# Performance work log

Measured on AMD Instinct MI355X. Metric: run time of the kernel, lower is better.

The kernel has to match this reference:

```python
import jax, jax.numpy as jnp
import numpy as np

B = 128      # batch
HW = 224     # image height/width
P = 16       # patch size
D = 512      # token_dim
NH = 8       # n_heads
L = 6        # t_blocks
M = 2048     # mlp_layer_size
NC = 10      # output classes
GP = HW // P            # patches per side
T = GP * GP + 1         # tokens incl. class token (197)
EPS = 1e-5


def _ln(x, g, b):
    m = jnp.mean(x, axis=-1, keepdims=True)
    v = jnp.mean(jnp.square(x - m), axis=-1, keepdims=True)
    return (x - m) / jnp.sqrt(v + EPS) * g + b


def setup_inputs() -> dict:
    key = jax.random.key(0)
    ks = iter(jax.random.split(key, 32))
    s = 0.02
    inp = {
        "images": jax.random.normal(next(ks), (B, 1, HW, HW), dtype=jnp.float32),
        "lin_map_w": jax.random.normal(next(ks), (D, P * P), dtype=jnp.float32) * s,
        "lin_map_b": jnp.zeros((D,), jnp.float32),
        "class_token": jax.random.uniform(next(ks), (1, D), dtype=jnp.float32),
        "ln1_g": jnp.ones((L, D), jnp.float32),
        "ln1_b": jnp.zeros((L, D), jnp.float32),
        "ln2_g": jnp.ones((L, D), jnp.float32),
        "ln2_b": jnp.zeros((L, D), jnp.float32),
        "qw": jax.random.normal(next(ks), (L, NH, D, D), dtype=jnp.float32) * s,
        "qb": jnp.zeros((L, NH, D), jnp.float32),
        "kw": jax.random.normal(next(ks), (L, NH, D, D), dtype=jnp.float32) * s,
        "kb": jnp.zeros((L, NH, D), jnp.float32),
        "vw": jax.random.normal(next(ks), (L, NH, D, D), dtype=jnp.float32) * s,
        "vb": jnp.zeros((L, NH, D), jnp.float32),
        "map_w": jax.random.normal(next(ks), (L, T, T * NH), dtype=jnp.float32) * s,
        "map_b": jnp.zeros((L, T), jnp.float32),
        "mlp_w1": jax.random.normal(next(ks), (L, M, D), dtype=jnp.float32) * s,
        "mlp_b1": jnp.zeros((L, M), jnp.float32),
        "mlp_w2": jax.random.normal(next(ks), (L, D, M), dtype=jnp.float32) * s,
        "mlp_b2": jnp.zeros((L, D), jnp.float32),
        "cls_w": jax.random.normal(next(ks), (NC, D), dtype=jnp.float32) * s,
        "cls_b": jnp.zeros((NC,), jnp.float32),
    }
    return inp


def reference(images, lin_map_w, lin_map_b, class_token, ln1_g, ln1_b, ln2_g, ln2_b,
              qw, qb, kw, kb, vw, vb, map_w, map_b,
              mlp_w1, mlp_b1, mlp_w2, mlp_b2, cls_w, cls_b):
    n = images.shape[0]
    img = images[:, 0]  # (B, HW, HW), channel squeezed as in patching_func
    # non-overlapping patch extraction (patchify with step=patch_size)
    patches = img.reshape(n, GP, P, GP, P).transpose(0, 1, 3, 2, 4).reshape(n, GP * GP, P * P)
    emb = patches @ lin_map_w.T + lin_map_b                 # (B, nP, D)
    cls = jnp.broadcast_to(class_token, (n, 1, D))
    x = jnp.concatenate([cls, emb], axis=1)                 # (B, T, D)
    scale = 1.0 / np.sqrt(T - 1)                            # quirky scale from source
    for l in range(L):
        h = _ln(x, ln1_g[l], ln1_b[l])
        q = jnp.einsum('btd,hed->bhte', h, qw[l]) + qb[l][None, :, None, :]
        k = jnp.einsum('btd,hed->bhte', h, kw[l]) + kb[l][None, :, None, :]
        v = jnp.einsum('btd,hed->bhte', h, vw[l]) + vb[l][None, :, None, :]
        attn = jax.nn.softmax(jnp.einsum('bhte,bhse->bhts', q, k) * scale, axis=-1)
        av = jnp.einsum('bhts,bhse->bhte', attn, v)         # (B, NH, T, D)
        res = av.reshape(n, NH * T, D)                      # head-major concat along tokens
        msa = jnp.einsum('bmd,tm->btd', res, map_w[l]) + map_b[l][None, :, None]
        x = x + msa
        y = _ln(x, ln2_g[l], ln2_b[l])
        mlp = jax.nn.gelu(y @ mlp_w1[l].T + mlp_b1[l], approximate=False) @ mlp_w2[l].T + mlp_b2[l]
        x = y + mlp                                         # note: residual uses ln2(x), per source
    logits = x[:, 0] @ cls_w.T + cls_b
    return jax.nn.softmax(logits, axis=-1)
```

## Files before the change

### kernel.cpp

```cpp
#include <hip/hip_runtime.h>
#include <hip/hip_bf16.h>
#include <math.h>

#define B_   128
#define HW_  224
#define P_   16
#define D_   512
#define NH_  8
#define L_   6
#define M_   2048
#define NC_  10
#define GP_  14
#define T_   197
#define TP_  224
#define EPS_ 1e-5f
#define ZVW2_ 2048
#define RCW_ 448

typedef __hip_bfloat16 bf16;
typedef __attribute__((ext_vector_type(8))) __bf16 bf16x8;
typedef __attribute__((ext_vector_type(4))) float  f32x4;

__device__ __forceinline__ void gload16(const void* g, void* l) {
    __builtin_amdgcn_global_load_lds(
        (const __attribute__((address_space(1))) void*)g,
        (__attribute__((address_space(3))) void*)l, 16, 0, 0);
}


__global__ void k_f32_to_bf16v(const float* __restrict__ in, bf16* __restrict__ out, long n8) {
    long stride = (long)gridDim.x * blockDim.x;
    for (long i = (long)blockIdx.x * blockDim.x + threadIdx.x; i < n8; i += stride) {
        float4 a = ((const float4*)in)[i * 2], b = ((const float4*)in)[i * 2 + 1];
        union { uint4 u; bf16 h[8]; } r;
        r.h[0] = __float2bfloat16(a.x); r.h[1] = __float2bfloat16(a.y);
        r.h[2] = __float2bfloat16(a.z); r.h[3] = __float2bfloat16(a.w);
        r.h[4] = __float2bfloat16(b.x); r.h[5] = __float2bfloat16(b.y);
        r.h[6] = __float2bfloat16(b.z); r.h[7] = __float2bfloat16(b.w);
        ((uint4*)out)[i] = r.u;
    }
}

__global__ void k_f32_to_bf16v2(const float* __restrict__ in1, bf16* __restrict__ out1,
                                const float* __restrict__ in2, bf16* __restrict__ out2, long n8) {
    long stride = (long)gridDim.x * blockDim.x;
    for (long i = (long)blockIdx.x * blockDim.x + threadIdx.x; i < n8; i += stride) {
        {
            float4 a = ((const float4*)in1)[i * 2], b = ((const float4*)in1)[i * 2 + 1];
            union { uint4 u; bf16 h[8]; } r;
            r.h[0] = __float2bfloat16(a.x); r.h[1] = __float2bfloat16(a.y);
            r.h[2] = __float2bfloat16(a.z); r.h[3] = __float2bfloat16(a.w);
            r.h[4] = __float2bfloat16(b.x); r.h[5] = __float2bfloat16(b.y);
            r.h[6] = __float2bfloat16(b.z); r.h[7] = __float2bfloat16(b.w);
            ((uint4*)out1)[i] = r.u;
        }
        {
            float4 a = ((const float4*)in2)[i * 2], b = ((const float4*)in2)[i * 2 + 1];
            union { uint4 u; bf16 h[8]; } r;
            r.h[0] = __float2bfloat16(a.x); r.h[1] = __float2bfloat16(a.y);
            r.h[2] = __float2bfloat16(a.z); r.h[3] = __float2bfloat16(a.w);
            r.h[4] = __float2bfloat16(b.x); r.h[5] = __float2bfloat16(b.y);
            r.h[6] = __float2bfloat16(b.z); r.h[7] = __float2bfloat16(b.w);
            ((uint4*)out2)[i] = r.u;
        }
    }
}

__global__ void k_prep_wv(const float* __restrict__ vw, bf16* __restrict__ wzv) {
    int idx = blockIdx.x * blockDim.x + threadIdx.x;
    if (idx >= NH_ * D_ * (D_ / 8)) return;
    int d8 = idx & 63;
    int e  = (idx >> 6) & 511;
    int h  = idx >> 15;
    long so = ((long)(h * D_ + e)) * D_ + d8 * 8;
    float4 a = *(const float4*)(vw + so), b = *(const float4*)(vw + so + 4);
    union { uint4 u; bf16 hh[8]; } rr;
    rr.hh[0] = __float2bfloat16(a.x); rr.hh[1] = __float2bfloat16(a.y);
    rr.hh[2] = __float2bfloat16(a.z); rr.hh[3] = __float2bfloat16(a.w);
    rr.hh[4] = __float2bfloat16(b.x); rr.hh[5] = __float2bfloat16(b.y);
    rr.hh[6] = __float2bfloat16(b.z); rr.hh[7] = __float2bfloat16(b.w);
    ((uint4*)wzv)[((long)(h * 1024 + 512 + e)) * 64 + d8] = rr.u;
}

__global__ void k_prep_ub(const float* __restrict__ kw, const float* __restrict__ qb,
                          const float* __restrict__ vb, float* __restrict__ out) {
    int idx = blockIdx.x * blockDim.x + threadIdx.x;
    if (idx >= NH_ * 1024) return;
    int j = idx & 1023, h = idx >> 10;
    if (j < 512) {
        const float* kwh = kw + (long)h * D_ * D_ + j;
        const float* qbh = qb + h * D_;
        float s = 0.f;
        for (int e = 0; e < D_; e++) s += kwh[(long)e * D_] * qbh[e];
        out[idx] = s;
    } else {
        out[idx] = vb[h * D_ + (j - 512)];
    }
}

__global__ void k_patchify(const float* __restrict__ img, bf16* __restrict__ patches) {
    long idx = (long)blockIdx.x * blockDim.x + threadIdx.x;
    long total = (long)B_ * 196 * 256;
    if (idx >= total) return;
    int q = (int)(idx & 255);
    int p = (int)((idx >> 8) % 196);
    int b = (int)(idx / (196 * 256));
    int gy = p / GP_, gx = p % GP_;
    int py = q >> 4,  px = q & 15;
    patches[idx] = __float2bfloat16(img[((long)b * HW_ + gy * P_ + py) * HW_ + gx * P_ + px]);
}

__global__ void k_cls_token(const float* __restrict__ tok, float* __restrict__ x) {
    int i = blockIdx.x * blockDim.x + threadIdx.x;
    if (i < B_ * D_) {
        int b = i >> 9, d = i & 511;
        x[(long)b * T_ * D_ + d] = tok[d];
    }
}

__global__ void k_prep_map(const float* __restrict__ in, bf16* __restrict__ out) {
    int idx = blockIdx.x * blockDim.x + threadIdx.x;
    int total = NH_ * T_ * TP_;
    if (idx >= total) return;
    int s = idx % TP_;
    int t = (idx / TP_) % T_;
    int h = idx / (TP_ * T_);
    float v = (s < T_) ? in[t * (T_ * NH_) + h * T_ + s] : 0.f;
    out[idx] = __float2bfloat16(v);
}


template<int WRITE_Y>
__global__ __launch_bounds__(256) void k_ln(const float* x,
        const float* __restrict__ g, const float* __restrict__ bb,
        bf16* __restrict__ obf, float* of, int rows) {
    int wid = blockIdx.x * 4 + (threadIdx.x >> 6);
    if (wid >= rows) return;
    int lane = threadIdx.x & 63;
    const float* xr = x + (long)wid * D_;
    float v[8];
    float s = 0.f;
#pragma unroll
    for (int i = 0; i < 8; i++) { v[i] = xr[i * 64 + lane]; s += v[i]; }
#pragma unroll
    for (int off = 32; off; off >>= 1) s += __shfl_xor(s, off, 64);
    float mean = s * (1.f / D_);
    float sq = 0.f;
#pragma unroll
    for (int i = 0; i < 8; i++) { float d = v[i] - mean; sq += d * d; }
#pragma unroll
    for (int off = 32; off; off >>= 1) sq += __shfl_xor(sq, off, 64);
    float inv = rsqrtf(sq * (1.f / D_) + EPS_);
#pragma unroll
    for (int i = 0; i < 8; i++) {
        int d = i * 64 + lane;
        float val = (v[i] - mean) * inv * g[d] + bb[d];
        obf[(long)wid * D_ + d] = __float2bfloat16(val);
        if (WRITE_Y) of[(long)wid * D_ + d] = val;
    }
}


__global__ __launch_bounds__(256) void k_attn_ssm2(
        const bf16* __restrict__ Qbase, long ldq, long qImg, long qHead,
        const bf16* __restrict__ Kbase, long ldk, long kImg,
        bf16* __restrict__ Pm, float scale) {
    __shared__ __align__(16) bf16 Qs[128][32];
    __shared__ __align__(16) bf16 Ks[256][32];
    int z = blockIdx.z;
    int img = z & 127, h2 = z >> 7;
    int q0 = blockIdx.y * 128;
    int tid = threadIdx.x;
    int wv = tid >> 6, lane = tid & 63;

    const bf16* Qp = Qbase + (long)img * qImg + (long)h2 * qHead;
    const bf16* Kp = Kbase + (long)img * kImg;

    int sRow = 16 * wv + (lane >> 2);
    int sCol = (lane & 3) * 8;
    const bf16* gQ = Qp + (long)(q0 + sRow) * ldq + sCol;
    const bf16* gK = Kp + (long)sRow * ldk + sCol;
    char* lQ = (char*)Qs + (16 * wv) * 64;
    char* lK = (char*)Ks + (16 * wv) * 64;

    f32x4 acc[2][13];
#pragma unroll
    for (int j = 0; j < 2; j++)
#pragma unroll
        for (int f = 0; f < 13; f++) acc[j][f] = (f32x4){0.f, 0.f, 0.f, 0.f};

    for (int kt = 0; kt < 16; kt++) {
        long k0 = (long)kt * 32;
        gload16(gQ + k0, lQ);
        gload16(gQ + 64 * ldq + k0, lQ + 4096);
#pragma unroll
        for (int p = 0; p < 4; p++)
            gload16(gK + (long)(p * 64) * ldk + k0, lK + p * 4096);
        __syncthreads();
        bf16x8 af[2];
#pragma unroll
        for (int j = 0; j < 2; j++)
            af[j] = *(const bf16x8*)&Qs[wv * 32 + j * 16 + (lane & 15)][(lane >> 4) * 8];
#pragma unroll
        for (int f = 0; f < 13; f++) {
            bf16x8 bfr = *(const bf16x8*)&Ks[f * 16 + (lane & 15)][(lane >> 4) * 8];
            acc[0][f] = __builtin_amdgcn_mfma_f32_16x16x32_bf16(af[0], bfr, acc[0][f], 0, 0, 0);
            acc[1][f] = __builtin_amdgcn_mfma_f32_16x16x32_bf16(af[1], bfr, acc[1][f], 0, 0, 0);
        }
        __syncthreads();
    }

    int c1 = lane & 15, grp = lane >> 4;
    const bf16 z0 = __float2bfloat16(0.f);
#pragma unroll
    for (int j = 0; j < 2; j++) {
        float mx[4] = {-1e30f, -1e30f, -1e30f, -1e30f};
        float sm[4] = {0.f, 0.f, 0.f, 0.f};
#pragma unroll
        for (int f = 0; f < 13; f++) {
            bool val = (f * 16 + c1 < T_);
#pragma unroll
            for (int r = 0; r < 4; r++) {
                float v = val ? acc[j][f][r] * scale : -1e30f;
                acc[j][f][r] = v;
                mx[r] = fmaxf(mx[r], v);
            }
        }
#pragma unroll
        for (int r = 0; r < 4; r++)
#pragma unroll
            for (int off = 1; off < 16; off <<= 1) mx[r] = fmaxf(mx[r], __shfl_xor(mx[r], off, 64));
#pragma unroll
        for (int f = 0; f < 13; f++) {
            bool val = (f * 16 + c1 < T_);
#pragma unroll
            for (int r = 0; r < 4; r++) {
                float e = val ? expf(acc[j][f][r] - mx[r]) : 0.f;
                acc[j][f][r] = e;
                sm[r] += e;
            }
        }
#pragma unroll
        for (int r = 0; r < 4; r++) {
#pragma unroll
            for (int off = 1; off < 16; off <<= 1) sm[r] += __shfl_xor(sm[r], off, 64);
            sm[r] = 1.f / sm[r];
        }
#pragma unroll
        for (int r = 0; r < 4; r++) {
            int qi = q0 + wv * 32 + j * 16 + grp * 4 + r;
            if (qi >= T_) continue;
            bf16* prow = Pm + ((long)z * T_ + qi) * TP_;
#pragma unroll
            for (int f = 0; f < 13; f++)
                prow[f * 16 + c1] = __float2bfloat16(acc[j][f][r] * sm[r]);
            prow[208 + c1] = z0;
        }
    }
}


__device__ __forceinline__ float geluf(float v) {
    return 0.5f * v * (1.f + erff(v * 0.70710678118654752f));
}

template<int MODE, bool GUARD, bool SWZ>
__global__ __launch_bounds__(256) void k_gemm_bt(
        const bf16* __restrict__ A, long lda, long bsA,
        const bf16* __restrict__ Bw, long ldb, long bsB,
        void* __restrict__ Cp, long ldc, long bsC,
        const float* __restrict__ bias,
        const float* res, long ldres,
        int Mt, int Nt, int Kt) {
    __shared__ __align__(16) bf16 As[128][32];
    __shared__ __align__(16) bf16 Bs[128][32];
    int bz = blockIdx.z;
    A  += (long)bz * bsA;
    Bw += (long)bz * bsB;

    unsigned bx = blockIdx.x, by = blockIdx.y;
    if (SWZ) {
        unsigned nx = gridDim.x;
        unsigned nwg = nx * gridDim.y;
        unsigned f = by * nx + bx;
        unsigned q = nwg >> 3, r = nwg & 7;
        unsigned xcd = f & 7, idx = f >> 3;
        unsigned base = (xcd < r) ? xcd * (q + 1) : r * (q + 1) + (xcd - r) * q;
        unsigned nf = base + idx;
        bx = nf % nx;
        by = nf / nx;
    }
    int m0 = by * 128, n0 = bx * 128;

    int tid = threadIdx.x;
    int wv = tid >> 6, lane = tid & 63;
    int wm = (wv >> 1) * 64, wn = (wv & 1) * 64;
    int lrow = lane & 15, koff = (lane >> 4) * 8;

    int rA = tid >> 2, pA = (tid & 3) * 8;
    const bf16* gA0 = A  + (long)(m0 + rA) * lda + pA;
    const bf16* gA1 = A  + (long)(m0 + 64 + rA) * lda + pA;
    const bf16* gB0 = Bw + (long)(n0 + rA) * ldb + pA;
    const bf16* gB1 = Bw + (long)(n0 + 64 + rA) * ldb + pA;
    char* lA0 = (char*)As + (wv * 64) * 16;
    char* lA1 = (char*)As + (256 + wv * 64) * 16;
    char* lB0 = (char*)Bs + (wv * 64) * 16;
    char* lB1 = (char*)Bs + (256 + wv * 64) * 16;

    f32x4 acc[4][4];
#pragma unroll
    for (int i = 0; i < 4; i++)
#pragma unroll
        for (int j = 0; j < 4; j++) acc[i][j] = (f32x4){0.f, 0.f, 0.f, 0.f};

    int kTiles = Kt >> 5;
    for (int kt = 0; kt < kTiles; kt++) {
        long k0 = (long)kt << 5;
        gload16(gA0 + k0, lA0);
        gload16(gA1 + k0, lA1);
        gload16(gB0 + k0, lB0);
        gload16(gB1 + k0, lB1);
        __syncthreads();
        bf16x8 af[4], bfr[4];
#pragma unroll
        for (int mi = 0; mi < 4; mi++) af[mi]  = *(const bf16x8*)&As[wm + mi * 16 + lrow][koff];
#pragma unroll
        for (int ni = 0; ni < 4; ni++) bfr[ni] = *(const bf16x8*)&Bs[wn + ni * 16 + lrow][koff];
#pragma unroll
        for (int mi = 0; mi < 4; mi++)
#pragma unroll
            for (int ni = 0; ni < 4; ni++)
                acc[mi][ni] = __builtin_amdgcn_mfma_f32_16x16x32_bf16(af[mi], bfr[ni], acc[mi][ni], 0, 0, 0);
        __syncthreads();
    }

    int r4 = (lane >> 4) * 4, c1 = lane & 15;
    float bv[4];
#pragma unroll
    for (int ni = 0; ni < 4; ni++) {
        int col = n0 + wn + ni * 16 + c1;
        bv[ni] = (bias && (!GUARD || col < Nt)) ? bias[col] : 0.f;
    }
#pragma unroll
    for (int mi = 0; mi < 4; mi++) {
#pragma unroll
        for (int r = 0; r < 4; r++) {
            int row = m0 + wm + mi * 16 + r4 + r;
            if (GUARD && row >= Mt) continue;
            long base = (long)bz * bsC + (long)row * ldc + n0 + wn + c1;
#pragma unroll
            for (int ni = 0; ni < 4; ni++) {
                if (GUARD && (n0 + wn + ni * 16 + c1) >= Nt) continue;
                float v = acc[mi][ni][r] + bv[ni];
                long cidx = base + ni * 16;
                if (MODE == 0)      ((float*)Cp)[cidx] = v;
                else if (MODE == 1) ((bf16*)Cp)[cidx]  = __float2bfloat16(v);
                else if (MODE == 2) ((bf16*)Cp)[cidx]  = __float2bfloat16(geluf(v));
                else                ((float*)Cp)[cidx] = v + res[(long)row * ldres + n0 + wn + c1 + ni * 16];
            }
        }
    }
}

__global__ __launch_bounds__(256) void k_gemm_r(
        const bf16* __restrict__ mapPair,
        const bf16* __restrict__ Pb,
        bf16* __restrict__ Rcat) {
    __shared__ __align__(16) bf16 As[128][32];
    __shared__ __align__(16) bf16 Bs[128][32];
    int z = blockIdx.z;
    int img = z & 127, h2 = z >> 7;
    const bf16* A  = mapPair + (long)h2 * T_ * TP_;
    const bf16* Bw = Pb + ((long)(h2 * 128 + img)) * (long)T_ * TP_;
    bf16* Cp = Rcat + (long)img * 224 * RCW_ + h2 * 224;
    int m0 = blockIdx.y * 128, n0 = blockIdx.x * 128;
    int tid = threadIdx.x;
    int wv = tid >> 6, lane = tid & 63;
    int wm = (wv >> 1) * 64, wn = (wv & 1) * 64;
    int lrow = lane & 15, koff = (lane >> 4) * 8;

    int rA = tid >> 2, pA = (tid & 3) * 8;
    const bf16* gA0 = A + (long)(m0 + rA) * TP_ + pA;
    const bf16* gA1 = A + (long)(m0 + 64 + rA) * TP_ + pA;
    char* lA0 = (char*)As + (wv * 64) * 16;
    char* lA1 = (char*)As + (256 + wv * 64) * 16;
    int bk = tid & 31, bg = tid >> 5;

    f32x4 acc[4][4];
#pragma unroll
    for (int i = 0; i < 4; i++)
#pragma unroll
        for (int j = 0; j < 4; j++) acc[i][j] = (f32x4){0.f, 0.f, 0.f, 0.f};

    for (int kt = 0; kt < 7; kt++) {
        long k0 = (long)kt << 5;
        gload16(gA0 + k0, lA0);
        gload16(gA1 + k0, lA1);
#pragma unroll
        for (int i = 0; i < 2; i++) {
            int g = bg + 8 * i;
            uint4 v = *(const uint4*)(Bw + (k0 + bk) * TP_ + n0 + g * 8);
            const bf16* pv = (const bf16*)&v;
#pragma unroll
            for (int j = 0; j < 8; j++) Bs[g * 8 + j][bk] = pv[j];
        }
        __syncthreads();
        bf16x8 af[4], bfr[4];
#pragma unroll
        for (int mi = 0; mi < 4; mi++) af[mi]  = *(const bf16x8*)&As[wm + mi * 16 + lrow][koff];
#pragma unroll
        for (int ni = 0; ni < 4; ni++) bfr[ni] = *(const bf16x8*)&Bs[wn + ni * 16 + lrow][koff];
#pragma unroll
        for (int mi = 0; mi < 4; mi++)
#pragma unroll
            for (int ni = 0; ni < 4; ni++)
                acc[mi][ni] = __builtin_amdgcn_mfma_f32_16x16x32_bf16(af[mi], bfr[ni], acc[mi][ni], 0, 0, 0);
        __syncthreads();
    }

    int r4 = (lane >> 4) * 4, c1 = lane & 15;
#pragma unroll
    for (int mi = 0; mi < 4; mi++) {
#pragma unroll
        for (int r = 0; r < 4; r++) {
            int row = m0 + wm + mi * 16 + r4 + r;
            if (row >= T_) continue;
#pragma unroll
            for (int ni = 0; ni < 4; ni++) {
                int col = n0 + wn + ni * 16 + c1;
                if (col >= 224) continue;
                Cp[(long)row * RCW_ + col] = __float2bfloat16(acc[mi][ni][r]);
            }
        }
    }
}

__global__ __launch_bounds__(256) void k_gemm_rv(
        const bf16* __restrict__ Rcat,
        const bf16* __restrict__ ZV,
        float* __restrict__ xf,
        const float* __restrict__ rowbias) {
    __shared__ __align__(16) bf16 As[128][32];
    __shared__ __align__(16) bf16 Bs[128][32];
    int img = blockIdx.z;
    const bf16* A = Rcat + (long)img * 224 * RCW_;
    const bf16* Vimg = ZV + (long)img * T_ * ZVW2_;
    float* Cp = xf + (long)img * T_ * D_;
    int m0 = blockIdx.y * 128, n0 = blockIdx.x * 128;
    int tid = threadIdx.x;
    int wv = tid >> 6, lane = tid & 63;
    int wm = (wv >> 1) * 64, wn = (wv & 1) * 64;
    int lrow = lane & 15, koff = (lane >> 4) * 8;

    int rA = tid >> 2, pA = (tid & 3) * 8;
    const bf16* gA0 = A + (long)(m0 + rA) * RCW_ + pA;
    const bf16* gA1 = A + (long)(m0 + 64 + rA) * RCW_ + pA;
    char* lA0 = (char*)As + (wv * 64) * 16;
    char* lA1 = (char*)As + (256 + wv * 64) * 16;
    int bk = tid & 31, bg = tid >> 5;

    f32x4 acc[4][4];
#pragma unroll
    for (int i = 0; i < 4; i++)
#pragma unroll
        for (int j = 0; j < 4; j++) acc[i][j] = (f32x4){0.f, 0.f, 0.f, 0.f};

    for (int kt = 0; kt < 14; kt++) {
        long k0 = (long)kt << 5;
        gload16(gA0 + k0, lA0);
        gload16(gA1 + k0, lA1);
        const bf16* Vb = (kt < 7) ? (Vimg + 512 + k0 * ZVW2_)
                                  : (Vimg + 1536 + (k0 - 224) * ZVW2_);
#pragma unroll
        for (int i = 0; i < 2; i++) {
            int g = bg + 8 * i;
            uint4 v = *(const uint4*)(Vb + (long)bk * ZVW2_ + n0 + g * 8);
            const bf16* pv = (const bf16*)&v;
#pragma unroll
            for (int j = 0; j < 8; j++) Bs[g * 8 + j][bk] = pv[j];
        }
        __syncthreads();
        bf16x8 af[4], bfr[4];
#pragma unroll
        for (int mi = 0; mi < 4; mi++) af[mi]  = *(const bf16x8*)&As[wm + mi * 16 + lrow][koff];
#pragma unroll
        for (int ni = 0; ni < 4; ni++) bfr[ni] = *(const bf16x8*)&Bs[wn + ni * 16 + lrow][koff];
#pragma unroll
        for (int mi = 0; mi < 4; mi++)
#pragma unroll
            for (int ni = 0; ni < 4; ni++)
                acc[mi][ni] = __builtin_amdgcn_mfma_f32_16x16x32_bf16(af[mi], bfr[ni], acc[mi][ni], 0, 0, 0);
        __syncthreads();
    }

    int r4 = (lane >> 4) * 4, c1 = lane & 15;
#pragma unroll
    for (int mi = 0; mi < 4; mi++) {
#pragma unroll
        for (int r = 0; r < 4; r++) {
            int row = m0 + wm + mi * 16 + r4 + r;
            if (row >= T_) continue;
            float rb = rowbias ? rowbias[row] : 0.f;
#pragma unroll
            for (int ni = 0; ni < 4; ni++) {
                int col = n0 + wn + ni * 16 + c1;
                Cp[(long)row * D_ + col] += acc[mi][ni][r] + rb * 0.25f;
            }
        }
    }
}

__global__ __launch_bounds__(256) void k_gemm_tn(
        const bf16* __restrict__ A, long lda, long bsA,
        const bf16* __restrict__ Bw, long ldb, long bsB,
        bf16* __restrict__ Cp, long ldc, long bsC,
        int Mt, int Nt, int Kt) {
    __shared__ __align__(16) bf16 As[128][32];
    __shared__ __align__(16) bf16 Bs[128][32];
    int bz = blockIdx.z;
    A  += (long)bz * bsA;
    Bw += (long)bz * bsB;
    int m0 = blockIdx.y * 128, n0 = blockIdx.x * 128;
    int tid = threadIdx.x;
    int wv = tid >> 6, lane = tid & 63;
    int wm = (wv >> 1) * 64, wn = (wv & 1) * 64;
    int lrow = lane & 15, koff = (lane >> 4) * 8;
    int bk = tid & 31, bg = tid >> 5;

    f32x4 acc[4][4];
#pragma unroll
    for (int i = 0; i < 4; i++)
#pragma unroll
        for (int j = 0; j < 4; j++) acc[i][j] = (f32x4){0.f, 0.f, 0.f, 0.f};

    int kTiles = Kt >> 5;
    for (int kt = 0; kt < kTiles; kt++) {
        long k0 = (long)kt << 5;
#pragma unroll
        for (int i = 0; i < 2; i++) {
            int g = bg + 8 * i;
            uint4 va = *(const uint4*)(A + (k0 + bk) * lda + m0 + g * 8);
            const bf16* pa = (const bf16*)&va;
#pragma unroll
            for (int j = 0; j < 8; j++) As[g * 8 + j][bk] = pa[j];
            uint4 vb = *(const uint4*)(Bw + (k0 + bk) * ldb + n0 + g * 8);
            const bf16* pb = (const bf16*)&vb;
#pragma unroll
            for (int j = 0; j < 8; j++) Bs[g * 8 + j][bk] = pb[j];
        }
        __syncthreads();
        bf16x8 af[4], bfr[4];
#pragma unroll
        for (int mi = 0; mi < 4; mi++) af[mi]  = *(const bf16x8*)&As[wm + mi * 16 + lrow][koff];
#pragma unroll
        for (int ni = 0; ni < 4; ni++) bfr[ni] = *(const bf16x8*)&Bs[wn + ni * 16 + lrow][koff];
#pragma unroll
        for (int mi = 0; mi < 4; mi++)
#pragma unroll
            for (int ni = 0; ni < 4; ni++)
                acc[mi][ni] = __builtin_amdgcn_mfma_f32_16x16x32_bf16(af[mi], bfr[ni], acc[mi][ni], 0, 0, 0);
        __syncthreads();
    }

    int r4 = (lane >> 4) * 4, c1 = lane & 15;
#pragma unroll
    for (int mi = 0; mi < 4; mi++) {
#pragma unroll
        for (int r = 0; r < 4; r++) {
            int row = m0 + wm + mi * 16 + r4 + r;
            if (row >= Mt) continue;
#pragma unroll
            for (int ni = 0; ni < 4; ni++) {
                int col = n0 + wn + ni * 16 + c1;
                if (col >= Nt) continue;
                Cp[(long)bz * bsC + (long)row * ldc + col] = __float2bfloat16(acc[mi][ni][r]);
            }
        }
    }
}


__global__ __launch_bounds__(64) void k_classifier(const float* __restrict__ x,
        const float* __restrict__ w, const float* __restrict__ bias, float* __restrict__ out) {
    int b = blockIdx.x, lane = threadIdx.x;
    const float* xr = x + (long)b * T_ * D_;
    float logits[NC_];
#pragma unroll
    for (int c = 0; c < NC_; c++) {
        float s = 0.f;
        for (int d = lane; d < D_; d += 64) s += xr[d] * w[c * D_ + d];
#pragma unroll
        for (int off = 32; off; off >>= 1) s += __shfl_xor(s, off, 64);
        logits[c] = s + bias[c];
    }
    float mx = -1e30f;
#pragma unroll
    for (int c = 0; c < NC_; c++) mx = fmaxf(mx, logits[c]);
    float sum = 0.f;
#pragma unroll
    for (int c = 0; c < NC_; c++) { float e = expf(logits[c] - mx); logits[c] = e; sum += e; }
    if (lane == 0) {
        float inv = 1.f / sum;
#pragma unroll
        for (int c = 0; c < NC_; c++) out[(long)b * NC_ + c] = logits[c] * inv;
    }
}


extern "C" void kernel_launch(void* const* d_in, const int* in_sizes, int n_in,
                              void* d_out, int out_size, void* d_ws, size_t ws_size,
                              hipStream_t stream) {
    const float* images  = (const float*)d_in[0];
    const float* lin_w   = (const float*)d_in[1];
    const float* lin_b   = (const float*)d_in[2];
    const float* cls_tok = (const float*)d_in[3];
    const float* ln1_g   = (const float*)d_in[4];
    const float* ln1_b   = (const float*)d_in[5];
    const float* ln2_g   = (const float*)d_in[6];
    const float* ln2_b   = (const float*)d_in[7];
    const float* qw      = (const float*)d_in[8];
    const float* qb      = (const float*)d_in[9];
    const float* kw      = (const float*)d_in[10];
    const float* kb      = (const float*)d_in[11];
    const float* vw      = (const float*)d_in[12];
    const float* vb      = (const float*)d_in[13];
    const float* map_w   = (const float*)d_in[14];
    const float* map_b   = (const float*)d_in[15];
    const float* w1      = (const float*)d_in[16];
    const float* b1      = (const float*)d_in[17];
    const float* w2      = (const float*)d_in[18];
    const float* b2      = (const float*)d_in[19];
    const float* cls_w   = (const float*)d_in[20];
    const float* cls_b   = (const float*)d_in[21];

    char* wp = (char*)d_ws;
    auto alloc = [&](size_t bytes) { char* p = wp; wp += (bytes + 255) & ~(size_t)255; return p; };
    const long BT = (long)B_ * T_;

    float* xf   = (float*)alloc(BT * D_ * 4);
    bf16*  hb   = (bf16*) alloc((BT + 192) * D_ * 2);
    bf16*  ZVh2 = (bf16*) alloc((size_t)(BT + 160) * ZVW2_ * 2);
    bf16*  m1c  = ZVh2;
    bf16*  Pb2  = (bf16*) alloc(((size_t)256 * T_ + 64) * TP_ * 2);
    char*  rcReg= alloc(((size_t)128 * 224 + 64) * RCW_ * 2);
    bf16*  Rcat = (bf16*)rcReg;
    bf16*  patches = (bf16*)rcReg;
    bf16*  wqb  = (bf16*)rcReg;
    bf16*  wkb  = (bf16*)(rcReg + (long)NH_ * D_ * D_ * 2);
    bf16*  wzv  = (bf16*) alloc(((long)NH_ * 1024 + 64) * D_ * 2);
    float* zvb  = (float*)alloc((long)NH_ * 1024 * 4);
    bf16*  wmapP= (bf16*) alloc(((long)NH_ * T_ + 64) * TP_ * 2);
    bf16*  w1l  = (bf16*) alloc((long)(M_ + 64) * D_ * 2);
    bf16*  w2l  = (bf16*) alloc((long)(D_ + 64) * M_ * 2);
    bf16*  wlin = (bf16*) alloc((long)(D_ + 64) * 256 * 2);

    k_f32_to_bf16v<<<1024, 256, 0, stream>>>(lin_w, wlin, (long)D_ * 256 / 8);
    {
        long tot = (long)B_ * 196 * 256;
        k_patchify<<<(int)((tot + 255) / 256), 256, 0, stream>>>(images, patches);
        k_cls_token<<<(B_ * D_ + 255) / 256, 256, 0, stream>>>(cls_tok, xf);
        k_gemm_bt<0, true, false><<<dim3(4, 2, B_), 256, 0, stream>>>(
            patches, 256, (long)196 * 256,
            wlin, 256, 0,
            xf + D_, D_, (long)T_ * D_,
            lin_b, nullptr, 0,
            196, D_, 256);
    }

    const float scale = 1.0f / 14.0f;
    const int lnGrid = (int)((BT + 3) / 4);

    for (int l = 0; l < L_; l++) {
        k_f32_to_bf16v2<<<1024, 256, 0, stream>>>(
            qw + (long)l * NH_ * D_ * D_, wqb,
            kw + (long)l * NH_ * D_ * D_, wkb, (long)NH_ * D_ * D_ / 8);
        k_gemm_tn<<<dim3(4, 4, NH_), 256, 0, stream>>>(
            wkb, D_, (long)D_ * D_,
            wqb, D_, (long)D_ * D_,
            wzv, D_, (long)1024 * D_,
            D_, D_, D_);
        k_prep_wv<<<(NH_ * D_ * (D_ / 8) + 255) / 256, 256, 0, stream>>>(
            vw + (long)l * NH_ * D_ * D_, wzv);
        k_prep_ub<<<(NH_ * 1024 + 255) / 256, 256, 0, stream>>>(
            kw + (long)l * NH_ * D_ * D_, qb + (long)l * NH_ * D_,
            vb + (long)l * NH_ * D_, zvb);
        k_f32_to_bf16v2<<<1024, 256, 0, stream>>>(
            w1 + (long)l * M_ * D_, w1l,
            w2 + (long)l * D_ * M_, w2l, (long)M_ * D_ / 8);
        k_prep_map<<<(NH_ * T_ * TP_ + 255) / 256, 256, 0, stream>>>(
            map_w + (long)l * T_ * T_ * NH_, wmapP);

        k_ln<0><<<lnGrid, 256, 0, stream>>>(xf, ln1_g + l * D_, ln1_b + l * D_, hb, nullptr, (int)BT);

        for (int hp = 0; hp < 4; hp++) {
            k_gemm_bt<1, false, true><<<dim3(16, 197, 1), 256, 0, stream>>>(
                hb, D_, 0, wzv + (long)hp * 2048 * D_, D_, 0,
                ZVh2, ZVW2_, 0, zvb + (long)hp * 2048, nullptr, 0,
                (int)BT, ZVW2_, D_);

            k_attn_ssm2<<<dim3(1, 2, 256), 256, 0, stream>>>(
                ZVh2, ZVW2_, (long)T_ * ZVW2_, 1024,
                hb, D_, (long)T_ * D_,
                Pb2, scale);

            k_gemm_r<<<dim3(2, 2, 256), 256, 0, stream>>>(
                wmapP + (long)(hp * 2) * T_ * TP_, Pb2, Rcat);

            k_gemm_rv<<<dim3(4, 2, B_), 256, 0, stream>>>(
                Rcat, ZVh2, xf, map_b + (long)l * T_);
        }

        k_ln<1><<<lnGrid, 256, 0, stream>>>(xf, ln2_g + l * D_, ln2_b + l * D_, hb, xf, (int)BT);

        k_gemm_bt<2, false, true><<<dim3(16, 197, 1), 256, 0, stream>>>(
            hb, D_, 0, w1l, D_, 0,
            m1c, M_, 0, b1 + (long)l * M_, nullptr, 0, (int)BT, M_, D_);
        k_gemm_bt<3, false, true><<<dim3(4, 197, 1), 256, 0, stream>>>(
            m1c, M_, 0, w2l, M_, 0,
            xf, D_, 0, b2 + (long)l * D_, xf, D_, (int)BT, D_, M_);
    }

    k_classifier<<<B_, 64, 0, stream>>>(xf, cls_w, cls_b, (float*)d_out);
}
```

Measured before the change: 7.700 ms.

## Add 256x256-tile double-buffered GEMM kernel for QKV and MLP projections

Introduces a new 512-thread GEMM kernel that uses 256x256 output tiles with K-step 64, double-buffered LDS filled via direct global-to-LDS loads, XOR-swizzled LDS layout, an XCD-aware workgroup remap, and s_setprio around the MFMA bursts. It replaces the older 128-tile GEMM for the Z/V projection, MLP up (GELU) and MLP down (residual) GEMMs. The larger tiles are meant to raise data reuse per tile and hide load latency. The M dimension is padded to 25344 rows with no bounds guard, so several buffers are enlarged to absorb out-of-range reads and writes. The bigger tile also reduces the number of workgroups and raises register and LDS pressure per block.

Result: slower. 8.166 ms (+6.0%).

```diff
diff --git a/kernel.cpp b/kernel.cpp
--- a/kernel.cpp
+++ b/kernel.cpp
@@ -16,6 +16,7 @@
 #define EPS_ 1e-5f
 #define ZVW2_ 2048
 #define RCW_ 448
+#define MPAD_ 25344
 
 typedef __hip_bfloat16 bf16;
 typedef __attribute__((ext_vector_type(8))) __bf16 bf16x8;
@@ -262,6 +263,113 @@
 
 __device__ __forceinline__ float geluf(float v) {
     return 0.5f * v * (1.f + erff(v * 0.70710678118654752f));
+}
+
+template<int MODE>
+__global__ __launch_bounds__(512, 2) void k_gemm_bt2(
+        const bf16* __restrict__ A, long lda,
+        const bf16* __restrict__ Bw, long ldb,
+        void* __restrict__ Cp, long ldc,
+        const float* __restrict__ bias,
+        const float* res, long ldres,
+        int Kt) {
+    __shared__ __align__(16) bf16 As[2][256][64];
+    __shared__ __align__(16) bf16 Bs[2][256][64];
+
+    unsigned bx = blockIdx.x, by = blockIdx.y;
+    {
+        unsigned nx = gridDim.x;
+        unsigned nwg = nx * gridDim.y;
+        unsigned f = by * nx + bx;
+        unsigned q = nwg >> 3, r = nwg & 7;
+        unsigned xcd = f & 7, idx = f >> 3;
+        unsigned base = (xcd < r) ? xcd * (q + 1) : r * (q + 1) + (xcd - r) * q;
+        unsigned nf = base + idx;
+        bx = nf % nx; by = nf / nx;
+    }
+    int m0 = by * 256, n0 = bx * 256;
+
+    int tid = threadIdx.x;
+    int wid = tid >> 6, lane = tid & 63;
+    int wm = (wid >> 2) * 128, wn = (wid & 3) * 64;
+    int lrow = lane & 15, kgrp = lane >> 4;
+
+    int rs = tid >> 3;
+    int csw = ((tid & 7) ^ ((tid >> 3) & 7)) << 3;
+    const bf16* gA = A  + (long)(m0 + rs) * lda + csw;
+    const bf16* gB = Bw + (long)(n0 + rs) * ldb + csw;
+    char* laB = (char*)As + wid * 1024;
+    char* lbB = (char*)Bs + wid * 1024;
+
+    f32x4 acc[8][4];
+#pragma unroll
+    for (int i = 0; i < 8; i++)
+#pragma unroll
+        for (int j = 0; j < 4; j++) acc[i][j] = (f32x4){0.f, 0.f, 0.f, 0.f};
+
+    auto stage = [&](int buf, int t) {
+        long k0 = (long)t << 6;
+#pragma unroll
+        for (int p = 0; p < 4; p++) {
+            gload16(gA + (long)(p * 64) * lda + k0, laB + buf * 32768 + p * 8192);
+            gload16(gB + (long)(p * 64) * ldb + k0, lbB + buf * 32768 + p * 8192);
+        }
+    };
+
+    int nt = Kt >> 6;
+    stage(0, 0);
+    __syncthreads();
+    int cur = 0;
+    for (int t = 0; t < nt; t++) {
+        stage(cur ^ 1, t + 1);
+        const bf16 (*Ac)[64] = As[cur];
+        const bf16 (*Bc)[64] = Bs[cur];
+#pragma unroll
+        for (int kk = 0; kk < 2; kk++) {
+            bf16x8 af[8], bfr[4];
+#pragma unroll
+            for (int mi = 0; mi < 8; mi++) {
+                int R = wm + mi * 16 + lrow;
+                af[mi] = *(const bf16x8*)&Ac[R][(((kk << 2) | kgrp) ^ (R & 7)) << 3];
+            }
+#pragma unroll
+            for (int ni = 0; ni < 4; ni++) {
+                int R = wn + ni * 16 + lrow;
+                bfr[ni] = *(const bf16x8*)&Bc[R][(((kk << 2) | kgrp) ^ (R & 7)) << 3];
+            }
+            __builtin_amdgcn_s_setprio(1);
+#pragma unroll
+            for (int mi = 0; mi < 8; mi++)
+#pragma unroll
+                for (int ni = 0; ni < 4; ni++)
+                    acc[mi][ni] = __builtin_amdgcn_mfma_f32_16x16x32_bf16(af[mi], bfr[ni], acc[mi][ni], 0, 0, 0);
+            __builtin_amdgcn_s_setprio(0);
+        }
+        __syncthreads();
+        cur ^= 1;
+    }
+
+    int r4 = (lane >> 4) * 4, c1 = lane & 15;
+    float bv[4];
+#pragma unroll
+    for (int ni = 0; ni < 4; ni++)
+        bv[ni] = bias ? bias[n0 + wn + ni * 16 + c1] : 0.f;
+#pragma unroll
+    for (int mi = 0; mi < 8; mi++) {
+#pragma unroll
+        for (int r = 0; r < 4; r++) {
+            long row = m0 + wm + mi * 16 + r4 + r;
+            long base = row * ldc + n0 + wn + c1;
+#pragma unroll
+            for (int ni = 0; ni < 4; ni++) {
+                float v = acc[mi][ni][r] + bv[ni];
+                long cidx = base + ni * 16;
+                if (MODE == 1)      ((bf16*)Cp)[cidx] = __float2bfloat16(v);
+                else if (MODE == 2) ((bf16*)Cp)[cidx] = __float2bfloat16(geluf(v));
+                else                ((float*)Cp)[cidx] = v + res[row * ldres + n0 + wn + c1 + ni * 16];
+            }
+        }
+    }
 }
 
 template<int MODE, bool GUARD, bool SWZ>
@@ -637,9 +745,9 @@
     auto alloc = [&](size_t bytes) { char* p = wp; wp += (bytes + 255) & ~(size_t)255; return p; };
     const long BT = (long)B_ * T_;
 
-    float* xf   = (float*)alloc(BT * D_ * 4);
+    float* xf   = (float*)alloc((BT + 192) * D_ * 4);
     bf16*  hb   = (bf16*) alloc((BT + 192) * D_ * 2);
-    bf16*  ZVh2 = (bf16*) alloc((size_t)(BT + 160) * ZVW2_ * 2);
+    bf16*  ZVh2 = (bf16*) alloc((size_t)(BT + 192) * ZVW2_ * 2);
     bf16*  m1c  = ZVh2;
     bf16*  Pb2  = (bf16*) alloc(((size_t)256 * T_ + 64) * TP_ * 2);
     char*  rcReg= alloc(((size_t)128 * 224 + 64) * RCW_ * 2);
@@ -647,11 +755,11 @@
     bf16*  patches = (bf16*)rcReg;
     bf16*  wqb  = (bf16*)rcReg;
     bf16*  wkb  = (bf16*)(rcReg + (long)NH_ * D_ * D_ * 2);
-    bf16*  wzv  = (bf16*) alloc(((long)NH_ * 1024 + 64) * D_ * 2);
+    bf16*  wzv  = (bf16*) alloc(((long)NH_ * 1024 + 320) * D_ * 2);
     float* zvb  = (float*)alloc((long)NH_ * 1024 * 4);
     bf16*  wmapP= (bf16*) alloc(((long)NH_ * T_ + 64) * TP_ * 2);
-    bf16*  w1l  = (bf16*) alloc((long)(M_ + 64) * D_ * 2);
-    bf16*  w2l  = (bf16*) alloc((long)(D_ + 64) * M_ * 2);
+    bf16*  w1l  = (bf16*) alloc((long)(M_ + 320) * D_ * 2);
+    bf16*  w2l  = (bf16*) alloc((long)(D_ + 320) * M_ * 2);
     bf16*  wlin = (bf16*) alloc((long)(D_ + 64) * 256 * 2);
 
     k_f32_to_bf16v<<<1024, 256, 0, stream>>>(lin_w, wlin, (long)D_ * 256 / 8);
@@ -693,10 +801,11 @@
         k_ln<0><<<lnGrid, 256, 0, stream>>>(xf, ln1_g + l * D_, ln1_b + l * D_, hb, nullptr, (int)BT);
 
         for (int hp = 0; hp < 4; hp++) {
-            k_gemm_bt<1, false, true><<<dim3(16, 197, 1), 256, 0, stream>>>(
-                hb, D_, 0, wzv + (long)hp * 2048 * D_, D_, 0,
-                ZVh2, ZVW2_, 0, zvb + (long)hp * 2048, nullptr, 0,
-                (int)BT, ZVW2_, D_);
+            k_gemm_bt2<1><<<dim3(8, MPAD_ / 256), 512, 0, stream>>>(
+                hb, D_,
+                wzv + (long)hp * 2048 * D_, D_,
+                ZVh2, ZVW2_,
+                zvb + (long)hp * 2048, nullptr, 0, D_);
 
             k_attn_ssm2<<<dim3(1, 2, 256), 256, 0, stream>>>(
                 ZVh2, ZVW2_, (long)T_ * ZVW2_, 1024,
@@ -712,12 +821,10 @@
 
         k_ln<1><<<lnGrid, 256, 0, stream>>>(xf, ln2_g + l * D_, ln2_b + l * D_, hb, xf, (int)BT);
 
-        k_gemm_bt<2, false, true><<<dim3(16, 197, 1), 256, 0, stream>>>(
-            hb, D_, 0, w1l, D_, 0,
-            m1c, M_, 0, b1 + (long)l * M_, nullptr, 0, (int)BT, M_, D_);
-        k_gemm_bt<3, false, true><<<dim3(4, 197, 1), 256, 0, stream>>>(
-            m1c, M_, 0, w2l, M_, 0,
-            xf, D_, 0, b2 + (long)l * D_, xf, D_, (int)BT, D_, M_);
+        k_gemm_bt2<2><<<dim3(8, MPAD_ / 256), 512, 0, stream>>>(
+            hb, D_, w1l, D_, m1c, M_, b1 + (long)l * M_, nullptr, 0, D_);
+        k_gemm_bt2<3><<<dim3(2, MPAD_ / 256), 512, 0, stream>>>(
+            m1c, M_, w2l, M_, xf, D_, b2 + (long)l * D_, xf, D_, M_);
     }
 
     k_classifier<<<B_, 64, 0, stream>>>(xf, cls_w, cls_b, (float*)d_out);
```
